# Kernel tuning notes

Hardware: AMD Instinct MI355X
Metric: run time of the kernel (lower is better)

Reference implementation:

```python
import jax, jax.numpy as jnp
import numpy as np

H, D = 8, 16  # heads, head_dim (hidden=128)
NEG_SLOPE = 0.2


def _seg_softmax(logits, seg, n):
    # softmax over edges grouped by destination node (leading axis)
    m = jax.ops.segment_max(logits, seg, num_segments=n)
    m = jnp.where(jnp.isfinite(m), m, 0.0)
    e = jnp.exp(logits - m[seg])
    s = jax.ops.segment_sum(e, seg, num_segments=n)
    return e / (s[seg] + 1e-16)


def _edge_type_out(x_src, x_dst, att_s, att_d, src, dst, n_dst):
    # GAT-style node-level attention for one edge type.
    # x_src: [Ns,H,D], x_dst: [Nd,H,D]
    a_s = (x_src * att_s).sum(-1)            # [Ns,H]
    a_d = (x_dst * att_d).sum(-1)            # [Nd,H]
    alpha = a_s[src] + a_d[dst]              # [E,H]
    alpha = jnp.where(alpha >= 0, alpha, NEG_SLOPE * alpha)  # leaky_relu(0.2)
    alpha = _seg_softmax(alpha, dst, n_dst)  # [E,H]
    msg = x_src[src] * alpha[:, :, None]     # [E,H,D]
    out = jax.ops.segment_sum(msg, dst, num_segments=n_dst)  # [Nd,H,D]
    return jax.nn.relu(out.reshape(n_dst, H * D))


def setup_inputs() -> dict:
    key = jax.random.key(0)
    ks = jax.random.split(key, 24)
    Na, Np, Nd = 300000, 150000, 80000
    E = 1000000
    hid = H * D
    inp = {
        "x_adm": jax.random.normal(ks[0], (Na, 128), jnp.float32),
        "x_pat": jax.random.normal(ks[1], (Np, 64), jnp.float32),
        "x_diag": jax.random.normal(ks[2], (Nd, 64), jnp.float32),
        "e_pa_src": jax.random.randint(ks[3], (E,), 0, Np),
        "e_pa_dst": jax.random.randint(ks[4], (E,), 0, Na),
        "e_da_src": jax.random.randint(ks[5], (E,), 0, Nd),
        "e_da_dst": jax.random.randint(ks[6], (E,), 0, Na),
        # per-node-type projections (PyG HANConv proj[node_type])
        "Wa": jax.random.normal(ks[7], (128, hid), jnp.float32) * 0.05,
        "ba": jnp.zeros((hid,), jnp.float32),
        "Wp": jax.random.normal(ks[8], (64, hid), jnp.float32) * 0.05,
        "bp": jnp.zeros((hid,), jnp.float32),
        "Wd": jax.random.normal(ks[9], (64, hid), jnp.float32) * 0.05,
        "bd": jnp.zeros((hid,), jnp.float32),
        # per-edge-type attention vectors [H,D]
        "ats_pa": jax.random.normal(ks[10], (H, D), jnp.float32) * 0.1,
        "atd_pa": jax.random.normal(ks[11], (H, D), jnp.float32) * 0.1,
        "ats_da": jax.random.normal(ks[12], (H, D), jnp.float32) * 0.1,
        "atd_da": jax.random.normal(ks[13], (H, D), jnp.float32) * 0.1,
        # semantic attention
        "Wk": jax.random.normal(ks[14], (hid, hid), jnp.float32) * 0.05,
        "bk": jnp.zeros((hid,), jnp.float32),
        "q": jax.random.normal(ks[15], (hid,), jnp.float32) * 0.1,
        # final classifier Linear(128, 2)
        "Wl": jax.random.normal(ks[16], (hid, 2), jnp.float32) * 0.05,
        "bl": jnp.zeros((2,), jnp.float32),
    }
    return inp


def reference(x_adm, x_pat, x_diag, e_pa_src, e_pa_dst, e_da_src, e_da_dst,
              Wa, ba, Wp, bp, Wd, bd,
              ats_pa, atd_pa, ats_da, atd_da,
              Wk, bk, q, Wl, bl):
    Na = x_adm.shape[0]
    h_a = (x_adm @ Wa + ba).reshape(Na, H, D)
    h_p = (x_pat @ Wp + bp).reshape(-1, H, D)
    h_d = (x_diag @ Wd + bd).reshape(-1, H, D)
    # node-level attention per metapath (dropout=0.6 skipped: eval mode)
    o_pa = _edge_type_out(h_p, h_a, ats_pa, atd_pa, e_pa_src, e_pa_dst, Na)
    o_da = _edge_type_out(h_d, h_a, ats_da, atd_da, e_da_src, e_da_dst, Na)
    # semantic-level attention across metapaths
    stack = jnp.stack([o_pa, o_da])                 # [2,Na,128]
    w = jnp.tanh(stack @ Wk + bk).mean(axis=1)      # [2,128]
    beta = jax.nn.softmax((w * q).sum(-1), axis=0)  # [2]
    sem = (beta[:, None, None] * stack).sum(0)      # [Na,128]
    logits = sem @ Wl + bl
    return jax.nn.softmax(logits, axis=1)
```

## Files before the change

### kernel.cpp

```cpp
#include <hip/hip_runtime.h>
#include <hip/hip_bf16.h>

typedef __hip_bfloat16 bf16;
typedef __attribute__((ext_vector_type(8))) short frag_ab;
typedef __attribute__((ext_vector_type(4))) float frag_cd;

__device__ __forceinline__ short f2bs(float f){
    bf16 h = __float2bfloat16(f); short s; __builtin_memcpy(&s, &h, 2); return s;
}
__device__ __forceinline__ unsigned pack2(float a, float b){
    return (unsigned)(unsigned short)f2bs(a) | (((unsigned)(unsigned short)f2bs(b)) << 16);
}
__device__ __forceinline__ float blo(unsigned u){ return __uint_as_float(u << 16); }
__device__ __forceinline__ float bhi(unsigned u){ return __uint_as_float(u & 0xffff0000u); }
__device__ __forceinline__ float fast_tanh(float x){
    x = fminf(fmaxf(x, -15.f), 15.f);
    const float t = __expf(2.f*x);
    return (t - 1.f) * __builtin_amdgcn_rcpf(t + 1.f);
}
static inline int imin(int a, int b){ return a < b ? a : b; }

__global__ void prep_fold(const float* __restrict__ Wa, const float* __restrict__ ba,
                          const float* __restrict__ atd_pa, const float* __restrict__ atd_da,
                          float* __restrict__ Wf, float* __restrict__ bdot)
{
    const int k = threadIdx.x;
    for (int g = 0; g < 16; g++){
        const float* att = (g < 8) ? atd_pa : atd_da;
        const int h = g & 7;
        float ssum = 0.f;
        for (int d = 0; d < 16; d++)
            ssum += Wa[k*128 + h*16 + d] * att[h*16 + d];
        Wf[k*16 + g] = ssum;
    }
    if (k < 16){
        const float* att = (k < 8) ? atd_pa : atd_da;
        const int h = k & 7;
        float sb = 0.f;
        for (int d = 0; d < 16; d++) sb += ba[h*16 + d] * att[h*16 + d];
        bdot[k] = sb;
    }
}

__global__ __launch_bounds__(256) void afold_kernel(
    const float* __restrict__ x,
    const float* __restrict__ Wf,
    const float* __restrict__ bdot,
    float* __restrict__ a_pa,
    float* __restrict__ a_da,
    int Na, int ntiles)
{
    __shared__ float WfT[16*132];
    __shared__ float xsr[16*132];
    __shared__ float bs[16];
    const int tid = threadIdx.x;
    for (int i = tid; i < 2048; i += 256){
        const int k = i >> 4, g = i & 15;
        WfT[g*132 + k] = Wf[k*16 + g];
    }
    if (tid < 16) bs[tid] = bdot[tid];
    const int r = tid >> 4, g = tid & 15;

    for (int tile = blockIdx.x; tile < ntiles; tile += gridDim.x){
        const int row0 = tile*16;
        __syncthreads();
        for (int i = tid; i < 512; i += 256){
            const int rr = i >> 5, c4 = (i & 31)*4;
            const int row = row0 + rr;
            float4 v = make_float4(0.f,0.f,0.f,0.f);
            if (row < Na) v = *(const float4*)&x[(size_t)row*128 + c4];
            *(float4*)&xsr[rr*132 + c4] = v;
        }
        __syncthreads();
        float acc = bs[g];
        #pragma unroll 4
        for (int k0 = 0; k0 < 128; k0 += 4){
            const float4 xv = *(const float4*)&xsr[r*132 + k0];
            const float4 wv = *(const float4*)&WfT[g*132 + k0];
            acc += xv.x*wv.x + xv.y*wv.y + xv.z*wv.z + xv.w*wv.w;
        }
        const int row = row0 + r;
        if (row < Na){
            if (g < 8) a_pa[(size_t)row*8 + g]     = acc;
            else       a_da[(size_t)row*8 + (g-8)] = acc;
        }
    }
}

__global__ __launch_bounds__(256) void proj64(
    const float* __restrict__ x,
    const float* __restrict__ W,
    const float* __restrict__ b,
    const float* __restrict__ att0,
    bf16*  __restrict__ h_out,
    float* __restrict__ a0_out,
    int N, int ntiles)
{
    constexpr int K = 64;
    __shared__ float Wsf[K*128];
    __shared__ float xs[32*K];
    const int tid = threadIdx.x;
    const int cg = tid & 31;
    const int rg = tid >> 5;

    for (int i = tid; i < K*32; i += 256)
        *(float4*)&Wsf[i*4] = *(const float4*)&W[i*4];

    float bc[4], at0v[4];
    #pragma unroll
    for (int u = 0; u < 4; u++){ bc[u] = b[cg*4+u]; at0v[u] = att0[cg*4+u]; }
    const int head = cg >> 2;

    for (int tile = blockIdx.x; tile < ntiles; tile += gridDim.x){
        const int row0 = tile*32;
        __syncthreads();
        for (int i = tid; i < 32*(K/4); i += 256){
            const int r  = i / (K/4);
            const int c4 = (i % (K/4))*4;
            const int row = row0 + r;
            float4 v = make_float4(0.f,0.f,0.f,0.f);
            if (row < N) v = *(const float4*)&x[(size_t)row*K + c4];
            *(float4*)&xs[r*K + c4] = v;
        }
        __syncthreads();

        float acc[4][4];
        #pragma unroll
        for (int j = 0; j < 4; j++){ acc[j][0]=acc[j][1]=acc[j][2]=acc[j][3]=0.f; }

        #pragma unroll 2
        for (int k0 = 0; k0 < K; k0 += 4){
            float xr[4][4];
            #pragma unroll
            for (int j = 0; j < 4; j++){
                const float4 v = *(const float4*)&xs[(rg*4+j)*K + k0];
                xr[j][0]=v.x; xr[j][1]=v.y; xr[j][2]=v.z; xr[j][3]=v.w;
            }
            #pragma unroll
            for (int kk = 0; kk < 4; kk++){
                const float4 wv = *(const float4*)&Wsf[(k0+kk)*128 + cg*4];
                #pragma unroll
                for (int j = 0; j < 4; j++){
                    acc[j][0] = fmaf(xr[j][kk], wv.x, acc[j][0]);
                    acc[j][1] = fmaf(xr[j][kk], wv.y, acc[j][1]);
                    acc[j][2] = fmaf(xr[j][kk], wv.z, acc[j][2]);
                    acc[j][3] = fmaf(xr[j][kk], wv.w, acc[j][3]);
                }
            }
        }

        #pragma unroll
        for (int j = 0; j < 4; j++){
            const int row = row0 + rg*4 + j;
            const bool valid = row < N;
            const float h0 = acc[j][0]+bc[0], h1 = acc[j][1]+bc[1];
            const float h2 = acc[j][2]+bc[2], h3 = acc[j][3]+bc[3];
            if (valid){
                h_out[(size_t)row*128 + cg*4+0] = __float2bfloat16(h0);
                h_out[(size_t)row*128 + cg*4+1] = __float2bfloat16(h1);
                h_out[(size_t)row*128 + cg*4+2] = __float2bfloat16(h2);
                h_out[(size_t)row*128 + cg*4+3] = __float2bfloat16(h3);
            }
            float p0 = h0*at0v[0] + h1*at0v[1] + h2*at0v[2] + h3*at0v[3];
            p0 += __shfl_down(p0, 2, 4);
            p0 += __shfl_down(p0, 1, 4);
            if (valid && (cg & 3) == 0) a0_out[(size_t)row*8 + head] = p0;
        }
    }
}

__global__ __launch_bounds__(256) void hist_kernel(
    const int* __restrict__ dst, int* __restrict__ cnt, int E)
{
    const int e = blockIdx.x*256 + threadIdx.x;
    if (e < E) atomicAdd(&cnt[dst[e]], 1);
}

__global__ __launch_bounds__(256) void scan_bsum(
    const int* __restrict__ cnt, int* __restrict__ bsum, int n)
{
    __shared__ int red[256];
    const int base = blockIdx.x*4096;
    int s = 0;
    for (int i = threadIdx.x; i < 4096; i += 256){
        const int idx = base + i;
        s += (idx < n) ? cnt[idx] : 0;
    }
    red[threadIdx.x] = s; __syncthreads();
    for (int st = 128; st > 0; st >>= 1){
        if (threadIdx.x < st) red[threadIdx.x] += red[threadIdx.x + st];
        __syncthreads();
    }
    if (threadIdx.x == 0) bsum[blockIdx.x] = red[0];
}

__global__ __launch_bounds__(256) void scan_excl(int* __restrict__ bsum, int nb)
{
    __shared__ int sh[256];
    const int t = threadIdx.x;
    sh[t] = (t < nb) ? bsum[t] : 0;
    __syncthreads();
    #pragma unroll
    for (int st = 1; st < 256; st <<= 1){
        const int u = (t >= st) ? sh[t - st] : 0;
        __syncthreads();
        sh[t] += u;
        __syncthreads();
    }
    if (t < nb) bsum[t] = t ? sh[t-1] : 0;
}

__global__ __launch_bounds__(256) void scan_write(
    int* __restrict__ cnt,
    const int* __restrict__ bsum,
    int* __restrict__ rowptr, int n)
{
    __shared__ int sh[256];
    const int t = threadIdx.x;
    const int base = blockIdx.x*4096 + t*16;
    int loc[16]; int s = 0;
    #pragma unroll
    for (int i = 0; i < 16; i += 4){
        int4 v = make_int4(0,0,0,0);
        if (base + i + 3 < n) v = *(const int4*)&cnt[base + i];
        else {
            if (base+i   < n) v.x = cnt[base+i];
            if (base+i+1 < n) v.y = cnt[base+i+1];
            if (base+i+2 < n) v.z = cnt[base+i+2];
            if (base+i+3 < n) v.w = cnt[base+i+3];
        }
        loc[i]   = s; s += v.x;
        loc[i+1] = s; s += v.y;
        loc[i+2] = s; s += v.z;
        loc[i+3] = s; s += v.w;
    }
    sh[t] = s; __syncthreads();
    #pragma unroll
    for (int st = 1; st < 256; st <<= 1){
        const int u = (t >= st) ? sh[t - st] : 0;
        __syncthreads();
        sh[t] += u;
        __syncthreads();
    }
    const int off = bsum[blockIdx.x] + (t ? sh[t-1] : 0);
    #pragma unroll
    for (int i = 0; i < 16; i++){
        const int idx = base + i;
        if (idx < n){
            const int v = off + loc[i];
            rowptr[idx] = v;
            cnt[idx]    = v;
        }
    }
    if (blockIdx.x == gridDim.x-1 && t == 255) rowptr[n] = off + s;
}

__global__ __launch_bounds__(256) void scatter_kernel(
    const int* __restrict__ src, const int* __restrict__ dst,
    int* __restrict__ cursor, int* __restrict__ sorted_src, int E)
{
    const int e = blockIdx.x*256 + threadIdx.x;
    if (e < E){
        const int pos = atomicAdd(&cursor[dst[e]], 1);
        sorted_src[pos] = src[e];
    }
}

#define GATHER_EDGE(Ax, Hx) { \
    float lg = (Ax) + ad; \
    lg = lg >= 0.f ? lg : 0.2f*lg; \
    lg = fminf(fmaxf(lg, -30.f), 30.f); \
    const float ee = __expf(lg); \
    acc0 = fmaf(ee, blo(Hx), acc0); \
    acc1 = fmaf(ee, bhi(Hx), acc1); \
    ssum += ee; }

__global__ __launch_bounds__(256) void gather_kernel(
    const int* __restrict__ rowptr, const int* __restrict__ sorted_src,
    const float* __restrict__ a_s,
    const float* __restrict__ a_d,
    const bf16*  __restrict__ h_src,
    unsigned* __restrict__ n_out,
    int Na)
{
    const int n = blockIdx.x*4 + (threadIdx.x >> 6);
    if (n >= Na) return;
    const int l = threadIdx.x & 63;
    const int h = l >> 3;
    const int beg = rowptr[n], end = rowptr[n+1];
    const float ad = a_d[(size_t)n*8 + h];
    const char* hb = (const char*)h_src;
    float acc0 = 0.f, acc1 = 0.f, ssum = 0.f;

    for (int base = beg; base < end; base += 64){
        const int nb = min(64, end - base);
        const int sv = sorted_src[min(base + l, end - 1)];
        for (int k = 0; k < nb; k += 4){
            const int r = nb - k;
            const int i0 = __shfl(sv, k);
            const int i1 = __shfl(sv, r > 1 ? k+1 : k);
            const int i2 = __shfl(sv, r > 2 ? k+2 : k);
            const int i3 = __shfl(sv, r > 3 ? k+3 : k);
            const float    A0 = a_s[(size_t)i0*8 + h];
            const unsigned H0 = *(const unsigned*)(hb + (size_t)i0*256 + l*4);
            const float    A1 = a_s[(size_t)i1*8 + h];
            const unsigned H1 = *(const unsigned*)(hb + (size_t)i1*256 + l*4);
            const float    A2 = a_s[(size_t)i2*8 + h];
            const unsigned H2 = *(const unsigned*)(hb + (size_t)i2*256 + l*4);
            const float    A3 = a_s[(size_t)i3*8 + h];
            const unsigned H3 = *(const unsigned*)(hb + (size_t)i3*256 + l*4);
            GATHER_EDGE(A0, H0)
            if (r > 1) GATHER_EDGE(A1, H1)
            if (r > 2) GATHER_EDGE(A2, H2)
            if (r > 3) GATHER_EDGE(A3, H3)
        }
    }
    const float inv = 1.f/(ssum + 1e-16f);
    n_out[(size_t)n*64 + l] = pack2(fmaxf(acc0*inv, 0.f), fmaxf(acc1*inv, 0.f));
}

__global__ __launch_bounds__(512) void semw_mfma(
    const unsigned* __restrict__ np, const unsigned* __restrict__ nd,
    const float* __restrict__ Wk, const float* __restrict__ bk,
    float* __restrict__ wsum, int Na, int ntiles)
{
    __shared__ short Bs[4*8*64*8];
    __shared__ short As[128*136];
    const int tid  = threadIdx.x;
    const int lane = tid & 63;
    const int w    = tid >> 6;
    const int quad = lane >> 4;
    const int m16  = lane & 15;
    const unsigned* __restrict__ nn = blockIdx.y ? nd : np;

    for (int f = tid; f < 4096; f += 512){
        const float4 v = *(const float4*)&Wk[f*4];
        const int k   = f >> 5;
        const int n4  = (f & 31)*4;
        const int k0i = k >> 5, kr = k & 31;
        const int lnb = (kr >> 3) << 4;
        const int j   = kr & 7;
        const float vv[4] = {v.x, v.y, v.z, v.w};
        #pragma unroll
        for (int t = 0; t < 4; t++){
            const int n = n4 + t;
            Bs[((k0i*8 + (n >> 4))*64 + (lnb | (n & 15)))*8 + j] = f2bs(vv[t]);
        }
    }

    float bkc[8];
    #pragma unroll
    for (int n0i = 0; n0i < 8; n0i++) bkc[n0i] = bk[n0i*16 + m16];

    float colsum[8] = {0.f,0.f,0.f,0.f,0.f,0.f,0.f,0.f};

    for (int tile = blockIdx.x; tile < ntiles; tile += gridDim.x){
        const int row0 = tile*128;
        __syncthreads();
        for (int i = tid; i < 2048; i += 512){
            const int r = i >> 4, c16 = i & 15;
            const int row = row0 + r;
            uint4 u = make_uint4(0,0,0,0);
            if (row < Na) u = *(const uint4*)&nn[(size_t)row*64 + c16*4];
            *(uint4*)&As[r*136 + c16*8] = u;
        }
        __syncthreads();

        frag_cd acc[8];
        #pragma unroll
        for (int n0i = 0; n0i < 8; n0i++) acc[n0i] = (frag_cd){0.f,0.f,0.f,0.f};

        #pragma unroll
        for (int k0i = 0; k0i < 4; k0i++){
            frag_ab av = *(const frag_ab*)&As[(w*16 + m16)*136 + k0i*32 + quad*8];
            #pragma unroll
            for (int n0i = 0; n0i < 8; n0i++){
                frag_ab bv = *(const frag_ab*)&Bs[((k0i*8 + n0i)*64 + lane)*8];
                acc[n0i] = __builtin_amdgcn_mfma_f32_16x16x32_bf16(av, bv, acc[n0i], 0, 0, 0);
            }
        }

        #pragma unroll
        for (int n0i = 0; n0i < 8; n0i++){
            float part = 0.f;
            #pragma unroll
            for (int r = 0; r < 4; r++){
                const int row = row0 + w*16 + quad*4 + r;
                if (row < Na) part += fast_tanh(acc[n0i][r] + bkc[n0i]);
            }
            part += __shfl_down(part, 32);
            part += __shfl_down(part, 16);
            if (lane < 16) colsum[n0i] += part;
        }
    }
    if (lane < 16){
        float* wdst = wsum + blockIdx.y*128;
        #pragma unroll
        for (int n0i = 0; n0i < 8; n0i++)
            unsafeAtomicAdd(&wdst[n0i*16 + lane], colsum[n0i]);
    }
}

__global__ void beta_kernel(const float* __restrict__ wsum, const float* __restrict__ q,
                            float* __restrict__ beta, float invN)
{
    __shared__ float r0s[128], r1s[128];
    const int tid = threadIdx.x;
    const float qv = q[tid];
    r0s[tid] = wsum[tid]     * invN * qv;
    r1s[tid] = wsum[128+tid] * invN * qv;
    __syncthreads();
    for (int st = 64; st > 0; st >>= 1){
        if (tid < st){ r0s[tid] += r0s[tid+st]; r1s[tid] += r1s[tid+st]; }
        __syncthreads();
    }
    if (tid == 0){
        const float w0 = r0s[0], w1 = r1s[0];
        const float m = fmaxf(w0, w1);
        const float e0 = __expf(w0-m), e1 = __expf(w1-m);
        const float inv = 1.f/(e0+e1);
        beta[0] = e0*inv; beta[1] = e1*inv;
    }
}

__global__ __launch_bounds__(256) void final_kernel(
    const unsigned* __restrict__ n_pa, const unsigned* __restrict__ n_da,
    const float* __restrict__ beta,
    const float* __restrict__ Wl, const float* __restrict__ bl,
    float* __restrict__ out, int Na)
{
    const int gtid = blockIdx.x*256 + threadIdx.x;
    const int node = gtid >> 6;
    const int lane = threadIdx.x & 63;
    if (node >= Na) return;
    const float b0 = beta[0], b1 = beta[1];
    const unsigned up = n_pa[(size_t)node*64 + lane];
    const unsigned ud = n_da[(size_t)node*64 + lane];
    const float sm0 = b0*blo(up) + b1*blo(ud);
    const float sm1 = b0*bhi(up) + b1*bhi(ud);
    const float4 wv = *(const float4*)&Wl[lane*4];
    float l0 = sm0*wv.x + sm1*wv.z;
    float l1 = sm0*wv.y + sm1*wv.w;
    #pragma unroll
    for (int off = 32; off > 0; off >>= 1){
        l0 += __shfl_down(l0, off);
        l1 += __shfl_down(l1, off);
    }
    if (lane == 0){
        l0 += bl[0]; l1 += bl[1];
        const float m = fmaxf(l0, l1);
        const float e0 = __expf(l0-m), e1 = __expf(l1-m);
        const float inv = 1.f/(e0+e1);
        out[(size_t)node*2+0] = e0*inv;
        out[(size_t)node*2+1] = e1*inv;
    }
}

extern "C" void kernel_launch(void* const* d_in, const int* in_sizes, int n_in,
                              void* d_out, int out_size, void* d_ws, size_t ws_size,
                              hipStream_t stream)
{
    const float* x_adm    = (const float*)d_in[0];
    const float* x_pat    = (const float*)d_in[1];
    const float* x_diag   = (const float*)d_in[2];
    const int*   e_pa_src = (const int*)d_in[3];
    const int*   e_pa_dst = (const int*)d_in[4];
    const int*   e_da_src = (const int*)d_in[5];
    const int*   e_da_dst = (const int*)d_in[6];
    const float* Wa = (const float*)d_in[7];
    const float* ba = (const float*)d_in[8];
    const float* Wp = (const float*)d_in[9];
    const float* bp = (const float*)d_in[10];
    const float* Wd = (const float*)d_in[11];
    const float* bd = (const float*)d_in[12];
    const float* ats_pa = (const float*)d_in[13];
    const float* atd_pa = (const float*)d_in[14];
    const float* ats_da = (const float*)d_in[15];
    const float* atd_da = (const float*)d_in[16];
    const float* Wk = (const float*)d_in[17];
    const float* bk = (const float*)d_in[18];
    const float* q  = (const float*)d_in[19];
    const float* Wl = (const float*)d_in[20];
    const float* bl = (const float*)d_in[21];

    const int Na  = in_sizes[0] / 128;
    const int Np  = in_sizes[1] / 64;
    const int Nd  = in_sizes[2] / 64;
    const int Epa = in_sizes[3];
    const int Eda = in_sizes[5];

    float* ws = (float*)d_ws;
    size_t off = 0;
    int*   cnt_pa = (int*)(ws + off); off += Na;
    int*   cnt_da = (int*)(ws + off); off += Na;
    float* wsum   = ws + off; off += 256;
    float* beta   = ws + off; off += 8;
    const size_t zero_len = off;
    off = (off + 3) & ~(size_t)3;
    unsigned* n_pa = (unsigned*)(ws + off); off += (size_t)Na*64;
    unsigned* n_da = (unsigned*)(ws + off); off += (size_t)Na*64;
    float* a_s_pa = ws + off; off += (size_t)Np*8;
    float* a_s_da = ws + off; off += (size_t)Nd*8;
    float* a_d_pa = ws + off; off += (size_t)Na*8;
    float* a_d_da = ws + off; off += (size_t)Na*8;
    float* Wf     = ws + off; off += 2048;
    float* bdot   = ws + off; off += 16;
    bf16*  h_p    = (bf16*)(ws + off); off += (size_t)Np*64;
    bf16*  h_d    = (bf16*)(ws + off); off += (size_t)Nd*64;
    int*   rowptr_pa = (int*)(ws + off); off += (size_t)Na + 1;
    int*   rowptr_da = (int*)(ws + off); off += (size_t)Na + 1;
    int*   sorted_pa = (int*)(ws + off); off += (size_t)Epa;
    int*   sorted_da = (int*)(ws + off); off += (size_t)Eda;
    int*   bsum_pa   = (int*)(ws + off); off += 256;
    int*   bsum_da   = (int*)(ws + off); off += 256;
    (void)n_in; (void)out_size; (void)ws_size; (void)off;

    hipMemsetAsync(d_ws, 0, zero_len*sizeof(float), stream);

    prep_fold<<<1,128,0,stream>>>(Wa, ba, atd_pa, atd_da, Wf, bdot);
    {
        const int nt = (Na + 15)/16;
        afold_kernel<<<imin(nt,4096),256,0,stream>>>(x_adm, Wf, bdot,
                                                     a_d_pa, a_d_da, Na, nt);
    }
    {
        const int nt = (Np + 31)/32;
        proj64<<<imin(nt,1024),256,0,stream>>>(x_pat, Wp, bp, ats_pa, h_p, a_s_pa, Np, nt);
    }
    {
        const int nt = (Nd + 31)/32;
        proj64<<<imin(nt,1024),256,0,stream>>>(x_diag, Wd, bd, ats_da, h_d, a_s_da, Nd, nt);
    }

    const int nbkt = (Na + 4095)/4096;
    hist_kernel<<<(Epa+255)/256, 256, 0, stream>>>(e_pa_dst, cnt_pa, Epa);
    hist_kernel<<<(Eda+255)/256, 256, 0, stream>>>(e_da_dst, cnt_da, Eda);
    scan_bsum<<<nbkt, 256, 0, stream>>>(cnt_pa, bsum_pa, Na);
    scan_bsum<<<nbkt, 256, 0, stream>>>(cnt_da, bsum_da, Na);
    scan_excl<<<1, 256, 0, stream>>>(bsum_pa, nbkt);
    scan_excl<<<1, 256, 0, stream>>>(bsum_da, nbkt);
    scan_write<<<nbkt, 256, 0, stream>>>(cnt_pa, bsum_pa, rowptr_pa, Na);
    scan_write<<<nbkt, 256, 0, stream>>>(cnt_da, bsum_da, rowptr_da, Na);
    scatter_kernel<<<(Epa+255)/256, 256, 0, stream>>>(e_pa_src, e_pa_dst, cnt_pa, sorted_pa, Epa);
    scatter_kernel<<<(Eda+255)/256, 256, 0, stream>>>(e_da_src, e_da_dst, cnt_da, sorted_da, Eda);

    gather_kernel<<<(Na+3)/4, 256, 0, stream>>>(rowptr_pa, sorted_pa,
                                                a_s_pa, a_d_pa, h_p, n_pa, Na);
    gather_kernel<<<(Na+3)/4, 256, 0, stream>>>(rowptr_da, sorted_da,
                                                a_s_da, a_d_da, h_d, n_da, Na);

    {
        const int nt = (Na + 127)/128;
        dim3 grid(imin(nt, 256), 2);
        semw_mfma<<<grid, 512, 0, stream>>>(n_pa, n_da, Wk, bk, wsum, Na, nt);
    }
    beta_kernel<<<1,128,0,stream>>>(wsum, q, beta, 1.f/(float)Na);

    final_kernel<<<(Na+3)/4, 256, 0, stream>>>(n_pa, n_da, beta,
                                               Wl, bl, (float*)d_out, Na);
}
```

Baseline: 975.4 us.

## Load semantic-attention A fragments directly from global with register prefetch

The semantic-weight MFMA kernel no longer stages node tiles through shared memory. Each wave now loads its A fragments straight from global into registers and prefetches the next tile while computing the current one. Blocks shrink to 256 threads on 64-row tiles with a larger grid, and per-wave column sums are reduced in shared memory before one atomic per column. This removes the per-tile LDS round trip and barriers, at the cost of more registers for the double-buffered fragments. The k-slice fragment mapping relies on the packed row layout matching the MFMA operand order.

```diff
diff --git a/kernel.cpp b/kernel.cpp
--- a/kernel.cpp
+++ b/kernel.cpp
@@ -319,13 +319,21 @@
     n_out[(size_t)n*64 + l] = pack2(fmaxf(acc0*inv, 0.f), fmaxf(acc1*inv, 0.f));
 }
 
-__global__ __launch_bounds__(512) void semw_mfma(
+#define SEMW_LOADA(dst, t) { \
+    const int row_  = (t)*64 + w*16 + m16; \
+    const size_t rb_ = (size_t)(row_ < Na ? row_ : Na-1)*64 + quad*4; \
+    dst##0 = *(const frag_ab*)&nn[rb_]; \
+    dst##1 = *(const frag_ab*)&nn[rb_ + 16]; \
+    dst##2 = *(const frag_ab*)&nn[rb_ + 32]; \
+    dst##3 = *(const frag_ab*)&nn[rb_ + 48]; }
+
+__global__ __launch_bounds__(256) void semw_mfma(
     const unsigned* __restrict__ np, const unsigned* __restrict__ nd,
     const float* __restrict__ Wk, const float* __restrict__ bk,
-    float* __restrict__ wsum, int Na, int ntiles)
+    float* __restrict__ wsum, int Na, int nt)
 {
     __shared__ short Bs[4*8*64*8];
-    __shared__ short As[128*136];
+    __shared__ float csum[4][8][16];
     const int tid  = threadIdx.x;
     const int lane = tid & 63;
     const int w    = tid >> 6;
@@ -333,7 +341,7 @@
     const int m16  = lane & 15;
     const unsigned* __restrict__ nn = blockIdx.y ? nd : np;
 
-    for (int f = tid; f < 4096; f += 512){
+    for (int f = tid; f < 4096; f += 256){
         const float4 v = *(const float4*)&Wk[f*4];
         const int k   = f >> 5;
         const int n4  = (f & 31)*4;
@@ -351,53 +359,59 @@
     float bkc[8];
     #pragma unroll
     for (int n0i = 0; n0i < 8; n0i++) bkc[n0i] = bk[n0i*16 + m16];
+    __syncthreads();
 
     float colsum[8] = {0.f,0.f,0.f,0.f,0.f,0.f,0.f,0.f};
 
-    for (int tile = blockIdx.x; tile < ntiles; tile += gridDim.x){
-        const int row0 = tile*128;
-        __syncthreads();
-        for (int i = tid; i < 2048; i += 512){
-            const int r = i >> 4, c16 = i & 15;
-            const int row = row0 + r;
-            uint4 u = make_uint4(0,0,0,0);
-            if (row < Na) u = *(const uint4*)&nn[(size_t)row*64 + c16*4];
-            *(uint4*)&As[r*136 + c16*8] = u;
-        }
-        __syncthreads();
+    int tile = blockIdx.x;
+    frag_ab a0 = {}, a1 = {}, a2 = {}, a3 = {};
+    frag_ab p0 = {}, p1 = {}, p2 = {}, p3 = {};
+    if (tile < nt) SEMW_LOADA(a, tile)
+    while (tile < nt){
+        const int tnext = tile + gridDim.x;
+        if (tnext < nt) SEMW_LOADA(p, tnext)
 
         frag_cd acc[8];
         #pragma unroll
         for (int n0i = 0; n0i < 8; n0i++) acc[n0i] = (frag_cd){0.f,0.f,0.f,0.f};
-
-        #pragma unroll
-        for (int k0i = 0; k0i < 4; k0i++){
-            frag_ab av = *(const frag_ab*)&As[(w*16 + m16)*136 + k0i*32 + quad*8];
-            #pragma unroll
-            for (int n0i = 0; n0i < 8; n0i++){
-                frag_ab bv = *(const frag_ab*)&Bs[((k0i*8 + n0i)*64 + lane)*8];
-                acc[n0i] = __builtin_amdgcn_mfma_f32_16x16x32_bf16(av, bv, acc[n0i], 0, 0, 0);
-            }
-        }
-
+        #pragma unroll
+        for (int n0i = 0; n0i < 8; n0i++){
+            acc[n0i] = __builtin_amdgcn_mfma_f32_16x16x32_bf16(a0,
+                *(const frag_ab*)&Bs[((0*8 + n0i)*64 + lane)*8], acc[n0i], 0, 0, 0);
+            acc[n0i] = __builtin_amdgcn_mfma_f32_16x16x32_bf16(a1,
+                *(const frag_ab*)&Bs[((1*8 + n0i)*64 + lane)*8], acc[n0i], 0, 0, 0);
+            acc[n0i] = __builtin_amdgcn_mfma_f32_16x16x32_bf16(a2,
+                *(const frag_ab*)&Bs[((2*8 + n0i)*64 + lane)*8], acc[n0i], 0, 0, 0);
+            acc[n0i] = __builtin_amdgcn_mfma_f32_16x16x32_bf16(a3,
+                *(const frag_ab*)&Bs[((3*8 + n0i)*64 + lane)*8], acc[n0i], 0, 0, 0);
+        }
+
+        const int row0 = tile*64 + w*16 + quad*4;
         #pragma unroll
         for (int n0i = 0; n0i < 8; n0i++){
             float part = 0.f;
             #pragma unroll
-            for (int r = 0; r < 4; r++){
-                const int row = row0 + w*16 + quad*4 + r;
-                if (row < Na) part += fast_tanh(acc[n0i][r] + bkc[n0i]);
-            }
+            for (int r = 0; r < 4; r++)
+                if (row0 + r < Na) part += fast_tanh(acc[n0i][r] + bkc[n0i]);
             part += __shfl_down(part, 32);
             part += __shfl_down(part, 16);
             if (lane < 16) colsum[n0i] += part;
         }
-    }
+
+        if (tnext < nt){ a0 = p0; a1 = p1; a2 = p2; a3 = p3; }
+        tile = tnext;
+    }
+
     if (lane < 16){
-        float* wdst = wsum + blockIdx.y*128;
-        #pragma unroll
-        for (int n0i = 0; n0i < 8; n0i++)
-            unsafeAtomicAdd(&wdst[n0i*16 + lane], colsum[n0i]);
+        #pragma unroll
+        for (int n0i = 0; n0i < 8; n0i++) csum[w][n0i][lane] = colsum[n0i];
+    }
+    __syncthreads();
+    if (tid < 128){
+        const int n0i = tid >> 4, l16 = tid & 15;
+        const float v = csum[0][n0i][l16] + csum[1][n0i][l16]
+                      + csum[2][n0i][l16] + csum[3][n0i][l16];
+        unsafeAtomicAdd(&wsum[blockIdx.y*128 + n0i*16 + l16], v);
     }
 }
 
@@ -550,9 +564,9 @@
                                                 a_s_da, a_d_da, h_d, n_da, Na);
 
     {
-        const int nt = (Na + 127)/128;
-        dim3 grid(imin(nt, 256), 2);
-        semw_mfma<<<grid, 512, 0, stream>>>(n_pa, n_da, Wk, bk, wsum, Na, nt);
+        const int nt = (Na + 63)/64;
+        dim3 grid(imin(nt, 512), 2);
+        semw_mfma<<<grid, 256, 0, stream>>>(n_pa, n_da, Wk, bk, wsum, Na, nt);
     }
     beta_kernel<<<1,128,0,stream>>>(wsum, q, beta, 1.f/(float)Na);
 
```

Measured after the change: 936.6 us. -4.0%, faster.
